# Kernel optimization log

Hardware: AMD Instinct MI355X
Metric: run time of the kernel (lower is better)

## Reference

```python
import jax, jax.numpy as jnp
import numpy as np

N_NODES = 100000
N_EDGES = 3200000
FEAT = 128
HID = 128
N_GRAPHS = 512


def setup_inputs() -> dict:
    key = jax.random.key(0)
    ks = jax.random.split(key, 16)
    x = jax.random.normal(ks[0], (N_NODES, FEAT), dtype=jnp.float32)
    edge_index = jax.random.randint(ks[1], (2, N_EDGES), 0, N_NODES, dtype=jnp.int32)
    edge_weight = jax.random.uniform(ks[2], (N_EDGES,), dtype=jnp.float32)
    batch = jnp.sort(jax.random.randint(ks[3], (N_NODES,), 0, N_GRAPHS, dtype=jnp.int32))
    s = 1.0 / np.sqrt(HID)
    W1 = jax.random.uniform(ks[4], (FEAT, HID), dtype=jnp.float32, minval=-s, maxval=s)
    W2 = jax.random.uniform(ks[5], (HID, HID), dtype=jnp.float32, minval=-s, maxval=s)
    W3 = jax.random.uniform(ks[6], (HID, HID), dtype=jnp.float32, minval=-s, maxval=s)
    W4 = jax.random.uniform(ks[7], (HID, HID), dtype=jnp.float32, minval=-s, maxval=s)
    b1 = jnp.zeros((HID,), jnp.float32)
    b2 = jnp.zeros((HID,), jnp.float32)
    b3 = jnp.zeros((HID,), jnp.float32)
    b4 = jnp.zeros((HID,), jnp.float32)
    Wc = jax.random.uniform(ks[8], (HID, 1), dtype=jnp.float32, minval=-s, maxval=s)
    bc = jnp.zeros((1,), jnp.float32)
    return dict(x=x, edge_index=edge_index, edge_weight=edge_weight, batch=batch,
                W1=W1, b1=b1, W2=W2, b2=b2, W3=W3, b3=b3, W4=W4, b4=b4, Wc=Wc, bc=bc)


def _gcn_norm(edge_index, edge_weight, n):
    # PyG gcn_norm with add_self_loops=True (self-loop weight 1)
    loop = jnp.arange(n, dtype=edge_index.dtype)
    src = jnp.concatenate([edge_index[0], loop])
    dst = jnp.concatenate([edge_index[1], loop])
    ew = jnp.concatenate([edge_weight, jnp.ones((n,), edge_weight.dtype)])
    deg = jax.ops.segment_sum(ew, dst, num_segments=n)
    dinv = jnp.where(deg > 0, jax.lax.rsqrt(jnp.maximum(deg, 1e-30)), 0.0)
    norm = dinv[src] * ew * dinv[dst]
    return src, dst, norm


def _gcn_conv(x, src, dst, norm, W, b, n):
    h = x @ W                      # [N, H] dense GEMM
    msg = h[src] * norm[:, None]   # [E+N, H] gather + scale
    out = jax.ops.segment_sum(msg, dst, num_segments=n)  # scatter-add
    return out + b


def reference(x, edge_index, edge_weight, batch,
              W1, b1, W2, b2, W3, b3, W4, b4, Wc, bc):
    n = x.shape[0]
    src, dst, norm = _gcn_norm(edge_index, edge_weight, n)
    h = jax.nn.relu(_gcn_conv(x, src, dst, norm, W1, b1, n))
    h = jax.nn.relu(_gcn_conv(h, src, dst, norm, W2, b2, n))
    h = jax.nn.relu(_gcn_conv(h, src, dst, norm, W3, b3, n))
    h = jax.nn.relu(_gcn_conv(h, src, dst, norm, W4, b4, n))
    # global mean pool over graphs
    sums = jax.ops.segment_sum(h, batch, num_segments=N_GRAPHS)
    cnt = jax.ops.segment_sum(jnp.ones((n,), h.dtype), batch, num_segments=N_GRAPHS)
    pooled = sums / jnp.maximum(cnt, 1.0)[:, None]
    return jax.nn.sigmoid(pooled @ Wc + bc)
```

## Files before the change

kernel.cpp:

```cpp
#include <hip/hip_runtime.h>
#include <math.h>


#define MASK40 ((1ull << 40) - 1)

typedef float v2f __attribute__((ext_vector_type(2)));

__device__ inline unsigned f2bf(float x) {
    unsigned u = __float_as_uint(x);
    return (u + 0x7FFFu + ((u >> 16) & 1u)) >> 16;
}

__global__ void init_packed(unsigned long long* packed, int n) {
    int i = blockIdx.x * blockDim.x + threadIdx.x;
    if (i < n) packed[i] = 0ull;
}

__global__ void edge_pass(const int* __restrict__ dst, const float* __restrict__ ew,
                          unsigned long long* packed, unsigned short* __restrict__ slot,
                          int E) {
    int e = blockIdx.x * blockDim.x + threadIdx.x;
    if (e < E) {
        int d = dst[e];
        unsigned int fx = (unsigned int)rintf(ew[e] * 16777216.0f);
        unsigned long long old =
            atomicAdd(&packed[d], (1ull << 40) | (unsigned long long)fx);
        slot[e] = (unsigned short)(old >> 40);
    }
}

__global__ void dinv_cnt_k(const unsigned long long* __restrict__ packed,
                           float* dinv, int* cnt, int n) {
    int i = blockIdx.x * blockDim.x + threadIdx.x;
    if (i < n) {
        unsigned long long p = packed[i];
        float deg = 1.0f + (float)(p & MASK40) * (1.0f / 16777216.0f);
        dinv[i] = rsqrtf(deg);
        cnt[i] = (int)(p >> 40);
    }
}

__global__ __launch_bounds__(1024) void scan1(const int* __restrict__ cnt, int* rowp,
                                              int* bsums, int total, int N) {
    __shared__ int sh[1024];
    int i = blockIdx.x * 1024 + threadIdx.x;
    int v = 0;
    if (i < N) v = cnt[i] + 1;
    sh[threadIdx.x] = v;
    __syncthreads();
    for (int off = 1; off < 1024; off <<= 1) {
        int t = (threadIdx.x >= (unsigned)off) ? sh[threadIdx.x - off] : 0;
        __syncthreads();
        sh[threadIdx.x] += t;
        __syncthreads();
    }
    if (i < total) rowp[i] = sh[threadIdx.x] - v;
    if (threadIdx.x == 1023) bsums[blockIdx.x] = sh[1023];
}

__global__ void scan2(int* bsums, int nb) {
    if (threadIdx.x == 0 && blockIdx.x == 0) {
        int run = 0;
        for (int b = 0; b < nb; ++b) { int t = bsums[b]; bsums[b] = run; run += t; }
    }
}

__global__ __launch_bounds__(1024) void scan3(int* rowp, const int* __restrict__ bsums,
                                              int total) {
    int i = blockIdx.x * 1024 + threadIdx.x;
    if (i < total) rowp[i] += bsums[blockIdx.x];
}

__global__ void selfloop_k(const int* __restrict__ rowp, const float* __restrict__ dinv,
                           int2* colval, int n) {
    int i = blockIdx.x * blockDim.x + threadIdx.x;
    if (i < n) {
        float dv = dinv[i];
        int2 cv;
        cv.x = i;
        cv.y = __float_as_int(dv * dv);
        colval[rowp[i]] = cv;
    }
}

__global__ void scatter2(const int* __restrict__ src, const int* __restrict__ dst,
                         const float* __restrict__ ew,
                         const unsigned short* __restrict__ slot,
                         const float* __restrict__ dinv, const int* __restrict__ rowp,
                         int2* colval, int E) {
    int e = blockIdx.x * blockDim.x + threadIdx.x;
    if (e < E) {
        int s = src[e], d = dst[e];
        int idx = rowp[d] + 1 + (int)slot[e];
        int2 cv;
        cv.x = s;
        cv.y = __float_as_int(dinv[s] * ew[e] * dinv[d]);
        colval[idx] = cv;
    }
}

template <int BF16IN>
__global__ __launch_bounds__(256) void gemm128(const void* __restrict__ Av,
                                               const float* __restrict__ W,
                                               unsigned* __restrict__ C, int n) {
    const int row = blockIdx.x * 256 + threadIdx.x;
    const int c0 = blockIdx.y * 32;
    if (row >= n) return;

    float acc[32];
#pragma unroll
    for (int j = 0; j < 32; ++j) acc[j] = 0.f;

    for (int kc = 0; kc < 4; ++kc) {
        float a[32];
        if (BF16IN) {
            const unsigned* Ar = (const unsigned*)Av + (size_t)row * 64 + kc * 16;
#pragma unroll
            for (int i = 0; i < 4; ++i) {
                uint4 u = *(const uint4*)&Ar[i * 4];
                a[i * 8 + 0] = __uint_as_float(u.x << 16);
                a[i * 8 + 1] = __uint_as_float(u.x & 0xFFFF0000u);
                a[i * 8 + 2] = __uint_as_float(u.y << 16);
                a[i * 8 + 3] = __uint_as_float(u.y & 0xFFFF0000u);
                a[i * 8 + 4] = __uint_as_float(u.z << 16);
                a[i * 8 + 5] = __uint_as_float(u.z & 0xFFFF0000u);
                a[i * 8 + 6] = __uint_as_float(u.w << 16);
                a[i * 8 + 7] = __uint_as_float(u.w & 0xFFFF0000u);
            }
        } else {
            const float* Ar = (const float*)Av + (size_t)row * 128 + kc * 32;
#pragma unroll
            for (int i = 0; i < 8; ++i) {
                float4 f = *(const float4*)&Ar[i * 4];
                a[i * 4 + 0] = f.x; a[i * 4 + 1] = f.y;
                a[i * 4 + 2] = f.z; a[i * 4 + 3] = f.w;
            }
        }
#pragma unroll
        for (int k4 = 0; k4 < 8; ++k4) {
            const float* Wk = W + (size_t)(kc * 32 + k4 * 4) * 128 + c0;
            const float a0 = a[k4 * 4 + 0], a1 = a[k4 * 4 + 1];
            const float a2 = a[k4 * 4 + 2], a3 = a[k4 * 4 + 3];
#pragma unroll
            for (int j = 0; j < 32; ++j) {
                acc[j] = fmaf(a0, Wk[j], acc[j]);
                acc[j] = fmaf(a1, Wk[128 + j], acc[j]);
                acc[j] = fmaf(a2, Wk[256 + j], acc[j]);
                acc[j] = fmaf(a3, Wk[384 + j], acc[j]);
            }
        }
    }

    unsigned* Cr = C + (size_t)row * 32 + blockIdx.y * 8;
#pragma unroll
    for (int i = 0; i < 2; ++i) {
        uint4 w;
        int d0 = __builtin_amdgcn_cvt_pk_fp8_f32(acc[i*16+ 0], acc[i*16+ 1], 0, false);
        d0     = __builtin_amdgcn_cvt_pk_fp8_f32(acc[i*16+ 2], acc[i*16+ 3], d0, true);
        int d1 = __builtin_amdgcn_cvt_pk_fp8_f32(acc[i*16+ 4], acc[i*16+ 5], 0, false);
        d1     = __builtin_amdgcn_cvt_pk_fp8_f32(acc[i*16+ 6], acc[i*16+ 7], d1, true);
        int d2 = __builtin_amdgcn_cvt_pk_fp8_f32(acc[i*16+ 8], acc[i*16+ 9], 0, false);
        d2     = __builtin_amdgcn_cvt_pk_fp8_f32(acc[i*16+10], acc[i*16+11], d2, true);
        int d3 = __builtin_amdgcn_cvt_pk_fp8_f32(acc[i*16+12], acc[i*16+13], 0, false);
        d3     = __builtin_amdgcn_cvt_pk_fp8_f32(acc[i*16+14], acc[i*16+15], d3, true);
        w.x = (unsigned)d0; w.y = (unsigned)d1; w.z = (unsigned)d2; w.w = (unsigned)d3;
        *(uint4*)&Cr[i * 4] = w;
    }
}

__global__ __launch_bounds__(64) void aggregate(const unsigned short* __restrict__ t8,
                                                const int* __restrict__ rowp,
                                                const int2* __restrict__ colval,
                                                const float* __restrict__ bias,
                                                unsigned* __restrict__ out16, int n) {
    const int v = blockIdx.x;
    const int lane = threadIdx.x;
    const int e0 = rowp[v], e1 = rowp[v + 1];
    float ax = 0.f, ay = 0.f;
    int e = e0;
    for (; e + 4 <= e1; e += 4) {
        const int2 cv0 = colval[e],     cv1 = colval[e + 1];
        const int2 cv2 = colval[e + 2], cv3 = colval[e + 3];
        const unsigned short u0 = t8[(size_t)cv0.x * 64 + lane];
        const unsigned short u1 = t8[(size_t)cv1.x * 64 + lane];
        const unsigned short u2 = t8[(size_t)cv2.x * 64 + lane];
        const unsigned short u3 = t8[(size_t)cv3.x * 64 + lane];
        const float w0 = __int_as_float(cv0.y), w1 = __int_as_float(cv1.y);
        const float w2 = __int_as_float(cv2.y), w3 = __int_as_float(cv3.y);
        const v2f h0 = __builtin_amdgcn_cvt_pk_f32_fp8((int)u0, false);
        const v2f h1 = __builtin_amdgcn_cvt_pk_f32_fp8((int)u1, false);
        const v2f h2 = __builtin_amdgcn_cvt_pk_f32_fp8((int)u2, false);
        const v2f h3 = __builtin_amdgcn_cvt_pk_f32_fp8((int)u3, false);
        ax = fmaf(w0, h0.x, ax); ay = fmaf(w0, h0.y, ay);
        ax = fmaf(w1, h1.x, ax); ay = fmaf(w1, h1.y, ay);
        ax = fmaf(w2, h2.x, ax); ay = fmaf(w2, h2.y, ay);
        ax = fmaf(w3, h3.x, ax); ay = fmaf(w3, h3.y, ay);
    }
    for (; e < e1; ++e) {
        const int2 cv = colval[e];
        const v2f hv = __builtin_amdgcn_cvt_pk_f32_fp8(
            (int)t8[(size_t)cv.x * 64 + lane], false);
        const float w = __int_as_float(cv.y);
        ax = fmaf(w, hv.x, ax); ay = fmaf(w, hv.y, ay);
    }
    const float2 b2 = *(const float2*)&bias[lane * 2];
    const float rx = fmaxf(ax + b2.x, 0.f);
    const float ry = fmaxf(ay + b2.y, 0.f);
    out16[(size_t)v * 64 + lane] = f2bf(rx) | (f2bf(ry) << 16);
}

__global__ __launch_bounds__(64) void aggregate_last(const unsigned short* __restrict__ t8,
                                                     const int* __restrict__ rowp,
                                                     const int2* __restrict__ colval,
                                                     const float* __restrict__ bias,
                                                     const float* __restrict__ Wc,
                                                     float* __restrict__ sv, int n) {
    const int v = blockIdx.x;
    const int lane = threadIdx.x;
    const int e0 = rowp[v], e1 = rowp[v + 1];
    float ax = 0.f, ay = 0.f;
    int e = e0;
    for (; e + 4 <= e1; e += 4) {
        const int2 cv0 = colval[e],     cv1 = colval[e + 1];
        const int2 cv2 = colval[e + 2], cv3 = colval[e + 3];
        const unsigned short u0 = t8[(size_t)cv0.x * 64 + lane];
        const unsigned short u1 = t8[(size_t)cv1.x * 64 + lane];
        const unsigned short u2 = t8[(size_t)cv2.x * 64 + lane];
        const unsigned short u3 = t8[(size_t)cv3.x * 64 + lane];
        const float w0 = __int_as_float(cv0.y), w1 = __int_as_float(cv1.y);
        const float w2 = __int_as_float(cv2.y), w3 = __int_as_float(cv3.y);
        const v2f h0 = __builtin_amdgcn_cvt_pk_f32_fp8((int)u0, false);
        const v2f h1 = __builtin_amdgcn_cvt_pk_f32_fp8((int)u1, false);
        const v2f h2 = __builtin_amdgcn_cvt_pk_f32_fp8((int)u2, false);
        const v2f h3 = __builtin_amdgcn_cvt_pk_f32_fp8((int)u3, false);
        ax = fmaf(w0, h0.x, ax); ay = fmaf(w0, h0.y, ay);
        ax = fmaf(w1, h1.x, ax); ay = fmaf(w1, h1.y, ay);
        ax = fmaf(w2, h2.x, ax); ay = fmaf(w2, h2.y, ay);
        ax = fmaf(w3, h3.x, ax); ay = fmaf(w3, h3.y, ay);
    }
    for (; e < e1; ++e) {
        const int2 cv = colval[e];
        const v2f hv = __builtin_amdgcn_cvt_pk_f32_fp8(
            (int)t8[(size_t)cv.x * 64 + lane], false);
        const float w = __int_as_float(cv.y);
        ax = fmaf(w, hv.x, ax); ay = fmaf(w, hv.y, ay);
    }
    const float2 b2 = *(const float2*)&bias[lane * 2];
    const float2 wc = *(const float2*)&Wc[lane * 2];
    float p = fmaxf(ax + b2.x, 0.f) * wc.x + fmaxf(ay + b2.y, 0.f) * wc.y;
#pragma unroll
    for (int off = 32; off; off >>= 1) p += __shfl_down(p, off);
    if (lane == 0) sv[v] = p;
}

__global__ void gstart_k(const int* __restrict__ batch, int* start, int N, int G) {
    int g = blockIdx.x * blockDim.x + threadIdx.x;
    if (g <= G) {
        int lo = 0, hi = N;
        while (lo < hi) {
            int mid = (lo + hi) >> 1;
            if (batch[mid] < g) lo = mid + 1; else hi = mid;
        }
        start[g] = lo;
    }
}

__global__ __launch_bounds__(256) void seg_pool(const float* __restrict__ sv,
                                                const int* __restrict__ start,
                                                const float* __restrict__ bc,
                                                float* __restrict__ out, int G) {
    __shared__ float sh[4];
    const int g = blockIdx.x;
    const int s = start[g], epos = start[g + 1];
    float acc = 0.f;
    for (int i = s + threadIdx.x; i < epos; i += 256) acc += sv[i];
#pragma unroll
    for (int off = 32; off; off >>= 1) acc += __shfl_down(acc, off);
    if ((threadIdx.x & 63) == 0) sh[threadIdx.x >> 6] = acc;
    __syncthreads();
    if (threadIdx.x == 0) {
        float sum = sh[0] + sh[1] + sh[2] + sh[3];
        float cnt = (float)(epos - s);
        float z = sum / fmaxf(cnt, 1.0f) + bc[0];
        out[g] = 1.0f / (1.0f + expf(-z));
    }
}

extern "C" void kernel_launch(void* const* d_in, const int* in_sizes, int n_in,
                              void* d_out, int out_size, void* d_ws, size_t ws_size,
                              hipStream_t stream) {
    const float* x   = (const float*)d_in[0];
    const int* ei    = (const int*)d_in[1];
    const float* ew  = (const float*)d_in[2];
    const int* batch = (const int*)d_in[3];
    const float* W1 = (const float*)d_in[4];  const float* b1 = (const float*)d_in[5];
    const float* W2 = (const float*)d_in[6];  const float* b2 = (const float*)d_in[7];
    const float* W3 = (const float*)d_in[8];  const float* b3 = (const float*)d_in[9];
    const float* W4 = (const float*)d_in[10]; const float* b4 = (const float*)d_in[11];
    const float* Wc = (const float*)d_in[12]; const float* bc = (const float*)d_in[13];

    const int N = in_sizes[0] / 128;
    const int E = in_sizes[2];
    const int G = out_size;
    const int* src = ei;
    const int* dst = ei + E;

    char* p = (char*)d_ws;
    auto alloc = [&](size_t bytes) {
        void* q = (void*)p;
        p += (bytes + 255) & ~(size_t)255;
        return q;
    };
    unsigned long long* packed = (unsigned long long*)alloc((size_t)N * 8);
    float* dinv = (float*)alloc((size_t)N * 4);
    int* cnt    = (int*)alloc((size_t)N * 4);
    unsigned short* slot = (unsigned short*)alloc((size_t)E * 2);
    int* rowp   = (int*)alloc((size_t)(N + 1) * 4);
    int* bsums  = (int*)alloc(1024 * 4);
    const size_t M = (size_t)E + (size_t)N;
    int2* colval = (int2*)alloc(M * 8);
    unsigned* tbuf = (unsigned*)alloc((size_t)N * 32 * 4);
    unsigned* hbuf = (unsigned*)alloc((size_t)N * 64 * 4);
    float* sv   = (float*)alloc((size_t)N * 4);
    int* start  = (int*)alloc((size_t)(G + 1) * 4);

    const int B = 256;
    init_packed<<<(N + B - 1) / B, B, 0, stream>>>(packed, N);
    edge_pass<<<(E + B - 1) / B, B, 0, stream>>>(dst, ew, packed, slot, E);
    dinv_cnt_k<<<(N + B - 1) / B, B, 0, stream>>>(packed, dinv, cnt, N);
    const int total = N + 1;
    const int nb = (total + 1023) / 1024;
    scan1<<<nb, 1024, 0, stream>>>(cnt, rowp, bsums, total, N);
    scan2<<<1, 64, 0, stream>>>(bsums, nb);
    scan3<<<nb, 1024, 0, stream>>>(rowp, bsums, total);
    selfloop_k<<<(N + B - 1) / B, B, 0, stream>>>(rowp, dinv, colval, N);
    scatter2<<<(E + B - 1) / B, B, 0, stream>>>(src, dst, ew, slot, dinv, rowp,
                                                colval, E);
    gstart_k<<<(G + 1 + B - 1) / B, B, 0, stream>>>(batch, start, N, G);

    const dim3 ggrid((N + 255) / 256, 4);
    const unsigned short* t8 = (const unsigned short*)tbuf;
    gemm128<0><<<ggrid, B, 0, stream>>>(x, W1, tbuf, N);
    aggregate<<<N, 64, 0, stream>>>(t8, rowp, colval, b1, hbuf, N);
    gemm128<1><<<ggrid, B, 0, stream>>>(hbuf, W2, tbuf, N);
    aggregate<<<N, 64, 0, stream>>>(t8, rowp, colval, b2, hbuf, N);
    gemm128<1><<<ggrid, B, 0, stream>>>(hbuf, W3, tbuf, N);
    aggregate<<<N, 64, 0, stream>>>(t8, rowp, colval, b3, hbuf, N);
    gemm128<1><<<ggrid, B, 0, stream>>>(hbuf, W4, tbuf, N);
    aggregate_last<<<N, 64, 0, stream>>>(t8, rowp, colval, b4, Wc, sv, N);

    seg_pool<<<G, B, 0, stream>>>(sv, start, bc, (float*)d_out, G);
}
```

Before: 959.9 us.

## Replace scalar FP32 GEMM with bf16 MFMA GEMM and permuted feature layout

Swaps the per-thread FMA dense transform for a kernel built on MFMA 16x16x32 bf16 instructions. To feed it, x is first converted to bf16 and the weights are pre-transposed and converted to bf16. Later-layer weights get a K permutation so the feature order the MFMA output produces lines up with what aggregate reads, and the bias and Wc indexing are remapped to match. This removes the large scalar FMA cost of the four GEMMs. In exchange it adds a conversion pass over x and rounds the first layer's input to bf16, and the permutation bookkeeping is easy to get wrong.

```diff
diff --git a/kernel.cpp b/kernel.cpp
--- a/kernel.cpp
+++ b/kernel.cpp
@@ -5,6 +5,8 @@
 #define MASK40 ((1ull << 40) - 1)
 
 typedef float v2f __attribute__((ext_vector_type(2)));
+typedef __bf16 bf16x8 __attribute__((ext_vector_type(8)));
+typedef float f32x4 __attribute__((ext_vector_type(4)));
 
 __device__ inline unsigned f2bf(float x) {
     unsigned u = __float_as_uint(x);
@@ -99,73 +101,72 @@
     }
 }
 
-template <int BF16IN>
-__global__ __launch_bounds__(256) void gemm128(const void* __restrict__ Av,
-                                               const float* __restrict__ W,
-                                               unsigned* __restrict__ C, int n) {
-    const int row = blockIdx.x * 256 + threadIdx.x;
-    const int c0 = blockIdx.y * 32;
-    if (row >= n) return;
-
-    float acc[32];
-#pragma unroll
-    for (int j = 0; j < 32; ++j) acc[j] = 0.f;
-
-    for (int kc = 0; kc < 4; ++kc) {
-        float a[32];
-        if (BF16IN) {
-            const unsigned* Ar = (const unsigned*)Av + (size_t)row * 64 + kc * 16;
-#pragma unroll
-            for (int i = 0; i < 4; ++i) {
-                uint4 u = *(const uint4*)&Ar[i * 4];
-                a[i * 8 + 0] = __uint_as_float(u.x << 16);
-                a[i * 8 + 1] = __uint_as_float(u.x & 0xFFFF0000u);
-                a[i * 8 + 2] = __uint_as_float(u.y << 16);
-                a[i * 8 + 3] = __uint_as_float(u.y & 0xFFFF0000u);
-                a[i * 8 + 4] = __uint_as_float(u.z << 16);
-                a[i * 8 + 5] = __uint_as_float(u.z & 0xFFFF0000u);
-                a[i * 8 + 6] = __uint_as_float(u.w << 16);
-                a[i * 8 + 7] = __uint_as_float(u.w & 0xFFFF0000u);
-            }
-        } else {
-            const float* Ar = (const float*)Av + (size_t)row * 128 + kc * 32;
-#pragma unroll
-            for (int i = 0; i < 8; ++i) {
-                float4 f = *(const float4*)&Ar[i * 4];
-                a[i * 4 + 0] = f.x; a[i * 4 + 1] = f.y;
-                a[i * 4 + 2] = f.z; a[i * 4 + 3] = f.w;
-            }
+__global__ void cvt_x(const float2* __restrict__ x, unsigned* __restrict__ xb,
+                      long n64) {
+    long t = (long)blockIdx.x * 256 + threadIdx.x;
+    if (t < n64) {
+        float2 f = x[t];
+        xb[t] = f2bf(f.x) | (f2bf(f.y) << 16);
+    }
+}
+
+__global__ void prep_w(const float* __restrict__ Wa, const float* __restrict__ Wb,
+                       const float* __restrict__ Wc, const float* __restrict__ Wd,
+                       unsigned short* __restrict__ Wt) {
+    const int l = blockIdx.y;
+    const float* W = (l == 0) ? Wa : (l == 1) ? Wb : (l == 2) ? Wc : Wd;
+    const int c = blockIdx.x, p = threadIdx.x;
+    int k;
+    if (l == 0) {
+        k = p;
+    } else {
+        int t = p >> 1, h = p & 1;
+        int i = t >> 2, s = (t >> 1) & 1, jj = 2 * (t & 1) + h;
+        k = 16 * (4 * s + jj) + i;
+    }
+    float v = W[k * 128 + c];
+    unsigned u = __float_as_uint(v);
+    Wt[l * 16384 + c * 128 + p] = (unsigned short)((u + 0x7FFFu + ((u >> 16) & 1u)) >> 16);
+}
+
+__global__ __launch_bounds__(256) void gemm_mfma(const uint4* __restrict__ A,
+                                                 const uint4* __restrict__ Wt,
+                                                 uint2* __restrict__ C) {
+    const int w = threadIdx.x >> 6;
+    const int lane = threadIdx.x & 63;
+    const int i = lane & 15, q = lane >> 4;
+    const long row_base = (long)blockIdx.x * 64 + w * 16;
+
+    f32x4 acc[8];
+#pragma unroll
+    for (int t = 0; t < 8; ++t) acc[t] = (f32x4){0.f, 0.f, 0.f, 0.f};
+
+    const uint4* Arow = A + (row_base + i) * 16 + q;
+#pragma unroll
+    for (int ks = 0; ks < 4; ++ks) {
+        const bf16x8 af = __builtin_bit_cast(bf16x8, Arow[ks * 4]);
+#pragma unroll
+        for (int ct = 0; ct < 8; ++ct) {
+            const bf16x8 bf = __builtin_bit_cast(
+                bf16x8, Wt[(size_t)(ct * 16 + i) * 16 + ks * 4 + q]);
+            acc[ct] = __builtin_amdgcn_mfma_f32_16x16x32_bf16(af, bf, acc[ct], 0, 0, 0);
         }
-#pragma unroll
-        for (int k4 = 0; k4 < 8; ++k4) {
-            const float* Wk = W + (size_t)(kc * 32 + k4 * 4) * 128 + c0;
-            const float a0 = a[k4 * 4 + 0], a1 = a[k4 * 4 + 1];
-            const float a2 = a[k4 * 4 + 2], a3 = a[k4 * 4 + 3];
-#pragma unroll
-            for (int j = 0; j < 32; ++j) {
-                acc[j] = fmaf(a0, Wk[j], acc[j]);
-                acc[j] = fmaf(a1, Wk[128 + j], acc[j]);
-                acc[j] = fmaf(a2, Wk[256 + j], acc[j]);
-                acc[j] = fmaf(a3, Wk[384 + j], acc[j]);
-            }
-        }
-    }
-
-    unsigned* Cr = C + (size_t)row * 32 + blockIdx.y * 8;
-#pragma unroll
-    for (int i = 0; i < 2; ++i) {
-        uint4 w;
-        int d0 = __builtin_amdgcn_cvt_pk_fp8_f32(acc[i*16+ 0], acc[i*16+ 1], 0, false);
-        d0     = __builtin_amdgcn_cvt_pk_fp8_f32(acc[i*16+ 2], acc[i*16+ 3], d0, true);
-        int d1 = __builtin_amdgcn_cvt_pk_fp8_f32(acc[i*16+ 4], acc[i*16+ 5], 0, false);
-        d1     = __builtin_amdgcn_cvt_pk_fp8_f32(acc[i*16+ 6], acc[i*16+ 7], d1, true);
-        int d2 = __builtin_amdgcn_cvt_pk_fp8_f32(acc[i*16+ 8], acc[i*16+ 9], 0, false);
-        d2     = __builtin_amdgcn_cvt_pk_fp8_f32(acc[i*16+10], acc[i*16+11], d2, true);
-        int d3 = __builtin_amdgcn_cvt_pk_fp8_f32(acc[i*16+12], acc[i*16+13], 0, false);
-        d3     = __builtin_amdgcn_cvt_pk_fp8_f32(acc[i*16+14], acc[i*16+15], d3, true);
-        w.x = (unsigned)d0; w.y = (unsigned)d1; w.z = (unsigned)d2; w.w = (unsigned)d3;
-        *(uint4*)&Cr[i * 4] = w;
-    }
+    }
+
+#pragma unroll
+    for (int reg = 0; reg < 4; ++reg) {
+        int d0 = __builtin_amdgcn_cvt_pk_fp8_f32(acc[0][reg], acc[1][reg], 0, false);
+        d0     = __builtin_amdgcn_cvt_pk_fp8_f32(acc[2][reg], acc[3][reg], d0, true);
+        int d1 = __builtin_amdgcn_cvt_pk_fp8_f32(acc[4][reg], acc[5][reg], 0, false);
+        d1     = __builtin_amdgcn_cvt_pk_fp8_f32(acc[6][reg], acc[7][reg], d1, true);
+        const long row = row_base + q * 4 + reg;
+        uint2 o; o.x = (unsigned)d0; o.y = (unsigned)d1;
+        C[row * 16 + i] = o;
+    }
+}
+
+__device__ inline int perm_f0(int lane) {
+    return 64 * ((lane >> 1) & 1) + 32 * (lane & 1) + (lane >> 2);
 }
 
 __global__ __launch_bounds__(64) void aggregate(const unsigned short* __restrict__ t8,
@@ -203,9 +204,9 @@
         const float w = __int_as_float(cv.y);
         ax = fmaf(w, hv.x, ax); ay = fmaf(w, hv.y, ay);
     }
-    const float2 b2 = *(const float2*)&bias[lane * 2];
-    const float rx = fmaxf(ax + b2.x, 0.f);
-    const float ry = fmaxf(ay + b2.y, 0.f);
+    const int f0 = perm_f0(lane);
+    const float rx = fmaxf(ax + bias[f0], 0.f);
+    const float ry = fmaxf(ay + bias[f0 + 16], 0.f);
     out16[(size_t)v * 64 + lane] = f2bf(rx) | (f2bf(ry) << 16);
 }
 
@@ -245,9 +246,9 @@
         const float w = __int_as_float(cv.y);
         ax = fmaf(w, hv.x, ax); ay = fmaf(w, hv.y, ay);
     }
-    const float2 b2 = *(const float2*)&bias[lane * 2];
-    const float2 wc = *(const float2*)&Wc[lane * 2];
-    float p = fmaxf(ax + b2.x, 0.f) * wc.x + fmaxf(ay + b2.y, 0.f) * wc.y;
+    const int f0 = perm_f0(lane);
+    float p = fmaxf(ax + bias[f0], 0.f) * Wc[f0] +
+              fmaxf(ay + bias[f0 + 16], 0.f) * Wc[f0 + 16];
 #pragma unroll
     for (int off = 32; off; off >>= 1) p += __shfl_down(p, off);
     if (lane == 0) sv[v] = p;
@@ -304,6 +305,8 @@
     const int G = out_size;
     const int* src = ei;
     const int* dst = ei + E;
+    const int nblk = (N + 63) / 64;
+    const long Npad = (long)nblk * 64;
 
     char* p = (char*)d_ws;
     auto alloc = [&](size_t bytes) {
@@ -319,8 +322,10 @@
     int* bsums  = (int*)alloc(1024 * 4);
     const size_t M = (size_t)E + (size_t)N;
     int2* colval = (int2*)alloc(M * 8);
-    unsigned* tbuf = (unsigned*)alloc((size_t)N * 32 * 4);
-    unsigned* hbuf = (unsigned*)alloc((size_t)N * 64 * 4);
+    unsigned* tbuf = (unsigned*)alloc((size_t)Npad * 32 * 4);
+    unsigned* hbuf = (unsigned*)alloc((size_t)Npad * 64 * 4);
+    unsigned* xb   = (unsigned*)alloc((size_t)Npad * 64 * 4);
+    unsigned short* Wt = (unsigned short*)alloc(4 * 16384 * 2);
     float* sv   = (float*)alloc((size_t)N * 4);
     int* start  = (int*)alloc((size_t)(G + 1) * 4);
 
@@ -338,15 +343,19 @@
                                                 colval, E);
     gstart_k<<<(G + 1 + B - 1) / B, B, 0, stream>>>(batch, start, N, G);
 
-    const dim3 ggrid((N + 255) / 256, 4);
+    const long n64 = (long)N * 64;
+    cvt_x<<<(int)((n64 + 255) / 256), B, 0, stream>>>((const float2*)x, xb, n64);
+    prep_w<<<dim3(128, 4), 128, 0, stream>>>(W1, W2, W3, W4, Wt);
+
     const unsigned short* t8 = (const unsigned short*)tbuf;
-    gemm128<0><<<ggrid, B, 0, stream>>>(x, W1, tbuf, N);
+    const uint4* Wt4 = (const uint4*)Wt;
+    gemm_mfma<<<nblk, B, 0, stream>>>((const uint4*)xb,   Wt4,         (uint2*)tbuf);
     aggregate<<<N, 64, 0, stream>>>(t8, rowp, colval, b1, hbuf, N);
-    gemm128<1><<<ggrid, B, 0, stream>>>(hbuf, W2, tbuf, N);
+    gemm_mfma<<<nblk, B, 0, stream>>>((const uint4*)hbuf, Wt4 + 2048,  (uint2*)tbuf);
     aggregate<<<N, 64, 0, stream>>>(t8, rowp, colval, b2, hbuf, N);
-    gemm128<1><<<ggrid, B, 0, stream>>>(hbuf, W3, tbuf, N);
+    gemm_mfma<<<nblk, B, 0, stream>>>((const uint4*)hbuf, Wt4 + 4096,  (uint2*)tbuf);
     aggregate<<<N, 64, 0, stream>>>(t8, rowp, colval, b3, hbuf, N);
-    gemm128<1><<<ggrid, B, 0, stream>>>(hbuf, W4, tbuf, N);
+    gemm_mfma<<<nblk, B, 0, stream>>>((const uint4*)hbuf, Wt4 + 6144,  (uint2*)tbuf);
     aggregate_last<<<N, 64, 0, stream>>>(t8, rowp, colval, b4, Wc, sv, N);
 
     seg_pool<<<G, B, 0, stream>>>(sv, start, bc, (float*)d_out, G);
```

Result: faster. 859.9 us (-10.4%).
